# Kernel tuning notes

Hardware: AMD Instinct MI355X
Metric: run time of the kernel (lower is better)

## Reference

```python
import jax, jax.numpy as jnp
import numpy as np

L, H, NH, NKV, HD, I, MAXS = 5, 1024, 16, 8, 128, 3072, 16
EPS = 1e-6
THETA = 1000000.0
N_REP = NH // NKV


def rms(x, w, eps=EPS):
    # RMSNorm over last dim (fp32 math as in the torch module)
    return w * (x * jax.lax.rsqrt(jnp.mean(x * x, axis=-1, keepdims=True) + eps))


def rotate_half(v):
    d = v.shape[-1] // 2
    return jnp.concatenate([-v[..., d:], v[..., :d]], axis=-1)


def setup_inputs() -> dict:
    key = jax.random.key(0)
    ks = jax.random.split(key, 20)
    s = 0.02
    inp = {
        'hidden_states': jax.random.normal(ks[0], (1, 1, H), jnp.float32),
        'position_id': jax.random.randint(ks[1], (1,), 0, MAXS, jnp.int64) if jax.config.jax_enable_x64 else jax.random.randint(ks[1], (1,), 0, MAXS).astype(jnp.int32),
        'past_keys': jax.random.normal(ks[2], (L, 1, NKV, MAXS, HD), jnp.float32),
        'past_values': jax.random.normal(ks[3], (L, 1, NKV, MAXS, HD), jnp.float32),
        'w_iln': jnp.ones((L, H), jnp.float32),
        'w_paln': jnp.ones((L, H), jnp.float32),
        'wq': jax.random.normal(ks[4], (L, NH * HD, H), jnp.float32) * s,
        'wk': jax.random.normal(ks[5], (L, NKV * HD, H), jnp.float32) * s,
        'wv': jax.random.normal(ks[6], (L, NKV * HD, H), jnp.float32) * s,
        'wo': jax.random.normal(ks[7], (L, H, NH * HD), jnp.float32) * s,
        'w_qn': jnp.ones((L, HD), jnp.float32),
        'w_kn': jnp.ones((L, HD), jnp.float32),
        'w_gate': jax.random.normal(ks[8], (L, I, H), jnp.float32) * s,
        'w_up': jax.random.normal(ks[9], (L, I, H), jnp.float32) * s,
        'w_down': jax.random.normal(ks[10], (L, H, I), jnp.float32) * s,
        'w_onorm': jnp.ones((H,), jnp.float32),
    }
    return inp


def reference(hidden_states, position_id, past_keys, past_values,
              w_iln, w_paln, wq, wk, wv, wo, w_qn, w_kn,
              w_gate, w_up, w_down, w_onorm):
    pos = position_id[0]
    # RoPE tables at the single decode position
    inv_freq = 1.0 / (THETA ** (jnp.arange(0, HD, 2, dtype=jnp.float32) / HD))  # [HD/2]
    freqs = pos.astype(jnp.float32) * inv_freq
    cos = jnp.concatenate([jnp.cos(freqs)] * 2)  # [HD]
    sin = jnp.concatenate([jnp.sin(freqs)] * 2)
    mask = jnp.arange(MAXS) > pos  # [MAXS] future positions masked
    scale = 1.0 / jnp.sqrt(jnp.float32(HD))

    x = hidden_states[0, 0]  # [H]

    def layer(x, xs):
        pk, pv, wi, wp, q_, k_, v_, o_, qn, kn, g_, u_, d_ = xs
        h = rms(x, wi)
        q = (q_ @ h).reshape(NH, HD)
        k_new = rms((k_ @ h).reshape(NKV, HD), kn)
        v_new = (v_ @ h).reshape(NKV, HD)
        q = rms(q, qn)
        q = q * cos + rotate_half(q) * sin
        k_new = k_new * cos + rotate_half(k_new) * sin
        # write new K/V at pos into the fixed-size cache
        kc = pk[0].at[:, pos, :].set(k_new)  # [NKV, MAXS, HD]
        vc = pv[0].at[:, pos, :].set(v_new)
        # GQA: repeat each kv head N_REP times (contiguous, matching torch expand)
        ke = jnp.repeat(kc, N_REP, axis=0)  # [NH, MAXS, HD]
        ve = jnp.repeat(vc, N_REP, axis=0)
        scores = jnp.einsum('hd,hkd->hk', q, ke) * scale
        scores = jnp.where(mask[None, :], -jnp.inf, scores)
        p = jax.nn.softmax(scores, axis=-1)
        attn = jnp.einsum('hk,hkd->hd', p, ve).reshape(NH * HD)
        x = x + o_ @ attn
        h = rms(x, wp)
        x = x + d_ @ (jax.nn.silu(g_ @ h) * (u_ @ h))
        return x, (kc[None], vc[None])

    xs = (past_keys, past_values, w_iln, w_paln, wq, wk, wv, wo,
          w_qn, w_kn, w_gate, w_up, w_down)
    x, (pks, pvs) = jax.lax.scan(layer, x, xs)
    out = rms(x, w_onorm)[None, None, :]  # [1,1,H]
    return out, pks, pvs


if __name__ == '__main__':
    o = reference(**setup_inputs())
    print(o[0].shape, o[1].shape, o[2].shape)
```

## Files before the change

kernel.cpp:

```cpp
#include <hip/hip_runtime.h>
#include <hip/hip_bf16.h>
#include <math.h>

typedef __hip_bfloat16 bf16;

#define L_    5
#define H_    1024
#define NH_   16
#define NKV_  8
#define HD_   128
#define I_    3072
#define MAXS_ 16
#define EPS_  1e-6f
#define KVE_  (L_ * NKV_ * MAXS_ * HD_)

static __device__ __forceinline__ float bl(unsigned u){ return __uint_as_float(u << 16); }
static __device__ __forceinline__ float bh(unsigned u){ return __uint_as_float(u & 0xffff0000u); }
static __device__ __forceinline__ float b2f(bf16 v){ return __bfloat162float(v); }

static __device__ __forceinline__ float wred(float v){
#pragma unroll
    for (int o = 32; o; o >>= 1) v += __shfl_xor(v, o, 64);
    return v;
}

static __device__ __forceinline__ float dot8(uint4 u, float4 a, float4 b){
    return bl(u.x)*a.x + bh(u.x)*a.y + bl(u.y)*a.z + bh(u.y)*a.w
         + bl(u.z)*b.x + bh(u.z)*b.y + bl(u.w)*b.z + bh(u.w)*b.w;
}

static __device__ __forceinline__ float rms_inv(float sumsq, float n){
    float a = sumsq / n + EPS_;
    float y = rsqrtf(a);
    y = y * (1.5f - 0.5f * a * y * y);
    return y;
}

static __device__ __forceinline__ float ld1(const void* p, size_t i, bool b16){
    return b16 ? b2f(((const bf16*)p)[i]) : ((const float*)p)[i];
}
static __device__ __forceinline__ void st1(void* p, size_t i, float v, bool b16){
    if (b16) ((bf16*)p)[i] = __float2bfloat16(v);
    else     ((float*)p)[i] = v;
}

static __device__ __forceinline__ float rowdot(const void* w, size_t off, int n,
                                               const float* hs, bool b16, int lane){
    float acc = 0.f;
    if (b16) {
        const uint4* wp = (const uint4*)((const ushort*)w + off);
#pragma unroll 6
        for (int c = 0; c < n / 512; c++) {
            uint4 u = wp[c * 64 + lane];
            const float4* h4 = (const float4*)&hs[c * 512 + lane * 8];
            acc += dot8(u, h4[0], h4[1]);
        }
    } else {
        const float4* wp = (const float4*)((const float*)w + off);
#pragma unroll 12
        for (int c = 0; c < n / 256; c++) {
            float4 u = wp[c * 64 + lane];
            float4 h = *(const float4*)&hs[c * 256 + lane * 4];
            acc += u.x * h.x + u.y * h.y + u.z * h.z + u.w * h.w;
        }
    }
    return acc;
}

__global__ void k_probe(const void* __restrict__ w_onorm, int* __restrict__ flag){
    if (threadIdx.x == 0 && blockIdx.x == 0)
        flag[0] = (((const ushort*)w_onorm)[0] == 0x3F80) ? 1 : 0;
}

__global__ __launch_bounds__(256) void k_init(const void* __restrict__ hid,
                                              const void* __restrict__ pk,
                                              const void* __restrict__ pv,
                                              const int* __restrict__ flag,
                                              float* __restrict__ x,
                                              void* __restrict__ out){
    bool b16 = flag[0] != 0;
    int i = blockIdx.x * 256 + threadIdx.x;
    if (i < H_) x[i] = ld1(hid, i, b16);
    if (b16) {
        const int NV = KVE_ / 8;
        if (i < NV) {
            ((uint4*)((bf16*)out + H_))[i]        = ((const uint4*)pk)[i];
            ((uint4*)((bf16*)out + H_ + KVE_))[i] = ((const uint4*)pv)[i];
        }
    } else {
        const int NV = KVE_ / 4;
        if (i < NV) {
            ((uint4*)((float*)out + H_))[i]        = ((const uint4*)pk)[i];
            ((uint4*)((float*)out + H_ + KVE_))[i] = ((const uint4*)pv)[i];
        }
    }
}

__global__ __launch_bounds__(256) void k_qkv(const float* __restrict__ x,
                                             const void* __restrict__ w_iln,
                                             const void* __restrict__ wq,
                                             const void* __restrict__ wk,
                                             const void* __restrict__ wv,
                                             const int* __restrict__ flag,
                                             float* __restrict__ qraw,
                                             float* __restrict__ kraw,
                                             float* __restrict__ vraw,
                                             int layer){
    __shared__ float hs[H_];
    __shared__ float red[4];
    bool b16 = flag[0] != 0;
    int tid = threadIdx.x, lane = tid & 63, wid = tid >> 6;

    float ss = 0.f;
    for (int j = tid; j < H_; j += 256) { float xv = x[j]; ss += xv * xv; hs[j] = xv; }
    ss = wred(ss);
    if (lane == 0) red[wid] = ss;
    __syncthreads();
    float inv = rms_inv(red[0] + red[1] + red[2] + red[3], (float)H_);
    for (int j = tid; j < H_; j += 256) hs[j] = hs[j] * inv * ld1(w_iln, (size_t)layer * H_ + j, b16);
    __syncthreads();

    for (int rr = wid; rr < 8; rr += 4) {
        int r = blockIdx.x * 8 + rr;
        const void* w; size_t off; float* dst;
        if (r < NH_ * HD_) {
            w = wq; off = (size_t)layer * NH_ * HD_ * H_ + (size_t)r * H_; dst = qraw + r;
        } else if (r < NH_ * HD_ + NKV_ * HD_) {
            int rk = r - NH_ * HD_;
            w = wk; off = (size_t)layer * NKV_ * HD_ * H_ + (size_t)rk * H_; dst = kraw + rk;
        } else {
            int rv = r - NH_ * HD_ - NKV_ * HD_;
            w = wv; off = (size_t)layer * NKV_ * HD_ * H_ + (size_t)rv * H_; dst = vraw + rv;
        }
        float acc = wred(rowdot(w, off, H_, hs, b16, lane));
        if (lane == 0) *dst = acc;
    }
}

__global__ __launch_bounds__(64) void k_rope(const float* __restrict__ qraw,
                                             const float* __restrict__ kraw,
                                             const float* __restrict__ vraw,
                                             const void* __restrict__ w_qn,
                                             const void* __restrict__ w_kn,
                                             const int* __restrict__ pos_p,
                                             const int* __restrict__ flag,
                                             float* __restrict__ qrot,
                                             void* __restrict__ out,
                                             int layer){
    bool b16 = flag[0] != 0;
    int b = blockIdx.x, lane = threadIdx.x;
    int pos = pos_p[0];
    pos = pos < 0 ? 0 : (pos > MAXS_ - 1 ? MAXS_ - 1 : pos);

    float fr = (float)pos * exp2f(-(float)lane * 0.31143075889569023f);
    float c = cosf(fr), s = sinf(fr);

    if (b < NH_) {
        int hh = b;
        float q0 = qraw[hh * HD_ + lane], q1 = qraw[hh * HD_ + 64 + lane];
        float inv = rms_inv(wred(q0 * q0 + q1 * q1), (float)HD_);
        q0 = q0 * inv * ld1(w_qn, (size_t)layer * HD_ + lane, b16);
        q1 = q1 * inv * ld1(w_qn, (size_t)layer * HD_ + 64 + lane, b16);
        qrot[hh * HD_ + lane]      = q0 * c - q1 * s;
        qrot[hh * HD_ + 64 + lane] = q1 * c + q0 * s;
    } else {
        int g = b - NH_;
        float k0 = kraw[g * HD_ + lane], k1 = kraw[g * HD_ + 64 + lane];
        float inv = rms_inv(wred(k0 * k0 + k1 * k1), (float)HD_);
        k0 = k0 * inv * ld1(w_kn, (size_t)layer * HD_ + lane, b16);
        k1 = k1 * inv * ld1(w_kn, (size_t)layer * HD_ + 64 + lane, b16);
        float k0r = k0 * c - k1 * s;
        float k1r = k1 * c + k0 * s;
        size_t kco = H_ + (size_t)layer * NKV_ * MAXS_ * HD_ + (size_t)g * MAXS_ * HD_;
        size_t vco = kco + KVE_;
        st1(out, kco + pos * HD_ + lane,      k0r, b16);
        st1(out, kco + pos * HD_ + 64 + lane, k1r, b16);
        st1(out, vco + pos * HD_ + lane,      vraw[g * HD_ + lane], b16);
        st1(out, vco + pos * HD_ + 64 + lane, vraw[g * HD_ + 64 + lane], b16);
    }
}

__global__ __launch_bounds__(64) void k_attn(const float* __restrict__ qrot,
                                             const int* __restrict__ pos_p,
                                             const int* __restrict__ flag,
                                             float* __restrict__ attn,
                                             const void* __restrict__ out,
                                             int layer){
    bool b16 = flag[0] != 0;
    int hh = blockIdx.x, lane = threadIdx.x, g = hh >> 1;
    int pos = pos_p[0];
    pos = pos < 0 ? 0 : (pos > MAXS_ - 1 ? MAXS_ - 1 : pos);

    size_t kco = H_ + (size_t)layer * NKV_ * MAXS_ * HD_ + (size_t)g * MAXS_ * HD_;
    size_t vco = kco + KVE_;

    float q0 = qrot[hh * HD_ + lane], q1 = qrot[hh * HD_ + 64 + lane];
    const float scale = 0.08838834764831845f;

    float sc[MAXS_];
    float m = -3.0e38f;
#pragma unroll
    for (int t = 0; t < MAXS_; t++) {
        float d = q0 * ld1(out, kco + t * HD_ + lane, b16)
                + q1 * ld1(out, kco + t * HD_ + 64 + lane, b16);
        d = wred(d) * scale;
        sc[t] = d;
        if (t <= pos) m = fmaxf(m, d);
    }
    float se = 0.f;
    float p[MAXS_];
#pragma unroll
    for (int t = 0; t < MAXS_; t++) {
        float e = (t <= pos) ? expf(sc[t] - m) : 0.0f;
        p[t] = e;
        se += e;
    }
    float rinv = 1.0f / se;
    float a0 = 0.f, a1 = 0.f;
#pragma unroll
    for (int t = 0; t < MAXS_; t++) {
        float pt = p[t] * rinv;
        a0 += pt * ld1(out, vco + t * HD_ + lane, b16);
        a1 += pt * ld1(out, vco + t * HD_ + 64 + lane, b16);
    }
    attn[hh * HD_ + lane]      = a0;
    attn[hh * HD_ + 64 + lane] = a1;
}

__global__ __launch_bounds__(256) void k_oproj(const float* __restrict__ attn,
                                               const void* __restrict__ wo,
                                               const int* __restrict__ flag,
                                               float* __restrict__ x,
                                               int layer){
    __shared__ float as_[NH_ * HD_];
    bool b16 = flag[0] != 0;
    int tid = threadIdx.x, lane = tid & 63, wid = tid >> 6;
    for (int j = tid; j < NH_ * HD_; j += 256) as_[j] = attn[j];
    __syncthreads();
    for (int rr = wid; rr < 8; rr += 4) {
        int r = blockIdx.x * 8 + rr;
        size_t off = (size_t)layer * H_ * NH_ * HD_ + (size_t)r * NH_ * HD_;
        float acc = wred(rowdot(wo, off, NH_ * HD_, as_, b16, lane));
        if (lane == 0) x[r] += acc;
    }
}

__global__ __launch_bounds__(256) void k_gateup(const float* __restrict__ x,
                                                const void* __restrict__ w_paln,
                                                const void* __restrict__ w_gate,
                                                const void* __restrict__ w_up,
                                                const int* __restrict__ flag,
                                                float* __restrict__ act,
                                                int layer){
    __shared__ float hs[H_];
    __shared__ float red[4];
    bool b16 = flag[0] != 0;
    int tid = threadIdx.x, lane = tid & 63, wid = tid >> 6;

    float ss = 0.f;
    for (int j = tid; j < H_; j += 256) { float xv = x[j]; ss += xv * xv; hs[j] = xv; }
    ss = wred(ss);
    if (lane == 0) red[wid] = ss;
    __syncthreads();
    float inv = rms_inv(red[0] + red[1] + red[2] + red[3], (float)H_);
    for (int j = tid; j < H_; j += 256) hs[j] = hs[j] * inv * ld1(w_paln, (size_t)layer * H_ + j, b16);
    __syncthreads();

    for (int pp = wid; pp < 8; pp += 4) {
        int i = blockIdx.x * 8 + pp;
        size_t off = (size_t)layer * I_ * H_ + (size_t)i * H_;
        float ag = wred(rowdot(w_gate, off, H_, hs, b16, lane));
        float au = wred(rowdot(w_up,   off, H_, hs, b16, lane));
        if (lane == 0) {
            float sig = 1.0f / (1.0f + expf(-ag));
            act[i] = ag * sig * au;
        }
    }
}

__global__ __launch_bounds__(256) void k_down(const float* __restrict__ act,
                                              const void* __restrict__ w_down,
                                              const int* __restrict__ flag,
                                              float* __restrict__ x,
                                              int layer){
    __shared__ float as_[I_];
    bool b16 = flag[0] != 0;
    int tid = threadIdx.x, lane = tid & 63, wid = tid >> 6;
    for (int j = tid; j < I_; j += 256) as_[j] = act[j];
    __syncthreads();
    for (int rr = wid; rr < 8; rr += 4) {
        int r = blockIdx.x * 8 + rr;
        size_t off = (size_t)layer * H_ * I_ + (size_t)r * I_;
        float acc = wred(rowdot(w_down, off, I_, as_, b16, lane));
        if (lane == 0) x[r] += acc;
    }
}

__global__ __launch_bounds__(256) void k_final(const float* __restrict__ x,
                                               const void* __restrict__ w_onorm,
                                               const int* __restrict__ flag,
                                               void* __restrict__ out){
    __shared__ float red[4];
    bool b16 = flag[0] != 0;
    int tid = threadIdx.x, lane = tid & 63, wid = tid >> 6;
    float ss = 0.f;
    for (int j = tid; j < H_; j += 256) { float xv = x[j]; ss += xv * xv; }
    ss = wred(ss);
    if (lane == 0) red[wid] = ss;
    __syncthreads();
    float inv = rms_inv(red[0] + red[1] + red[2] + red[3], (float)H_);
    for (int j = tid; j < H_; j += 256)
        st1(out, j, x[j] * inv * ld1(w_onorm, j, b16), b16);
}

extern "C" void kernel_launch(void* const* d_in, const int* in_sizes, int n_in,
                              void* d_out, int out_size, void* d_ws, size_t ws_size,
                              hipStream_t stream) {
    const void* hid     = d_in[0];
    const int*  pos     = (const int*)d_in[1];
    const void* pk      = d_in[2];
    const void* pv      = d_in[3];
    const void* w_iln   = d_in[4];
    const void* w_paln  = d_in[5];
    const void* wq      = d_in[6];
    const void* wk      = d_in[7];
    const void* wv      = d_in[8];
    const void* wo      = d_in[9];
    const void* w_qn    = d_in[10];
    const void* w_kn    = d_in[11];
    const void* w_gate  = d_in[12];
    const void* w_up    = d_in[13];
    const void* w_down  = d_in[14];
    const void* w_onorm = d_in[15];

    float* ws   = (float*)d_ws;
    int*   flag = (int*)ws;
    float* x    = ws + 16;
    float* qraw = x + 1024;
    float* kraw = qraw + 2048;
    float* vraw = kraw + 1024;
    float* qrot = vraw + 1024;
    float* attn = qrot + 2048;
    float* act  = attn + 2048;

    k_probe<<<1, 64, 0, stream>>>(w_onorm, flag);
    k_init<<<80, 256, 0, stream>>>(hid, pk, pv, flag, x, d_out);
    for (int l = 0; l < L_; l++) {
        k_qkv<<<512, 256, 0, stream>>>(x, w_iln, wq, wk, wv, flag, qraw, kraw, vraw, l);
        k_rope<<<24, 64, 0, stream>>>(qraw, kraw, vraw, w_qn, w_kn, pos, flag, qrot, d_out, l);
        k_attn<<<16, 64, 0, stream>>>(qrot, pos, flag, attn, d_out, l);
        k_oproj<<<128, 256, 0, stream>>>(attn, wo, flag, x, l);
        k_gateup<<<384, 256, 0, stream>>>(x, w_paln, w_gate, w_up, flag, act, l);
        k_down<<<128, 256, 0, stream>>>(act, w_down, flag, x, l);
    }
    k_final<<<1, 256, 0, stream>>>(x, w_onorm, flag, d_out);
}
```

Before: 475.3 us.

## Fuse all decode layers into one cooperative persistent kernel with grid syncs

```diff
diff --git a/kernel.cpp b/kernel.cpp
--- a/kernel.cpp
+++ b/kernel.cpp
@@ -1,7 +1,9 @@
 #include <hip/hip_runtime.h>
+#include <hip/hip_cooperative_groups.h>
 #include <hip/hip_bf16.h>
 #include <math.h>
 
+namespace cg = cooperative_groups;
 typedef __hip_bfloat16 bf16;
 
 #define L_    5
@@ -49,7 +51,6 @@
     float acc = 0.f;
     if (b16) {
         const uint4* wp = (const uint4*)((const ushort*)w + off);
-#pragma unroll 6
         for (int c = 0; c < n / 512; c++) {
             uint4 u = wp[c * 64 + lane];
             const float4* h4 = (const float4*)&hs[c * 512 + lane * 8];
@@ -57,7 +58,6 @@
         }
     } else {
         const float4* wp = (const float4*)((const float*)w + off);
-#pragma unroll 12
         for (int c = 0; c < n / 256; c++) {
             float4 u = wp[c * 64 + lane];
             float4 h = *(const float4*)&hs[c * 256 + lane * 4];
@@ -65,6 +65,193 @@
         }
     }
     return acc;
+}
+
+struct MArgs {
+    const void *hid, *pk, *pv, *w_iln, *w_paln, *wq, *wk, *wv, *wo;
+    const void *w_qn, *w_kn, *w_gate, *w_up, *w_down, *w_onorm;
+    const int* pos;
+    float *x, *qraw, *kraw, *vraw, *attn, *act;
+    void* out;
+};
+
+__global__ __launch_bounds__(256, 2) void k_mega(MArgs a){
+    cg::grid_group grid = cg::this_grid();
+    __shared__ float smem[I_];
+    __shared__ float red4[4];
+    __shared__ float pA[16], pB[16];
+    const bool b16 = (((const ushort*)a.w_onorm)[0] == 0x3F80);
+    const int tid = threadIdx.x, lane = tid & 63, wid = tid >> 6;
+    const int b = blockIdx.x;
+    const int gsz = gridDim.x * 256, gtid = b * 256 + tid;
+    int pos = a.pos[0]; pos = pos < 0 ? 0 : (pos > MAXS_ - 1 ? MAXS_ - 1 : pos);
+
+    for (int i = gtid; i < H_; i += gsz) a.x[i] = ld1(a.hid, i, b16);
+    if (b16) {
+        uint4* ko = (uint4*)((bf16*)a.out + H_);
+        uint4* vo = (uint4*)((bf16*)a.out + H_ + KVE_);
+        for (int i = gtid; i < KVE_ / 8; i += gsz) { ko[i] = ((const uint4*)a.pk)[i]; vo[i] = ((const uint4*)a.pv)[i]; }
+    } else {
+        uint4* ko = (uint4*)((float*)a.out + H_);
+        uint4* vo = (uint4*)((float*)a.out + H_ + KVE_);
+        for (int i = gtid; i < KVE_ / 4; i += gsz) { ko[i] = ((const uint4*)a.pk)[i]; vo[i] = ((const uint4*)a.pv)[i]; }
+    }
+    grid.sync();
+
+    for (int l = 0; l < L_; l++) {
+        {
+            float ss = 0.f;
+            for (int j = tid; j < H_; j += 256) { float xv = a.x[j]; ss += xv * xv; smem[j] = xv; }
+            ss = wred(ss);
+            if (lane == 0) red4[wid] = ss;
+            __syncthreads();
+            float inv = rms_inv(red4[0] + red4[1] + red4[2] + red4[3], (float)H_);
+            for (int j = tid; j < H_; j += 256) smem[j] = smem[j] * inv * ld1(a.w_iln, (size_t)l * H_ + j, b16);
+            __syncthreads();
+            for (int rr = wid; rr < 8; rr += 4) {
+                int r = b * 8 + rr;
+                const void* w; size_t off; float* dst;
+                if (r < NH_ * HD_) {
+                    w = a.wq; off = (size_t)l * NH_ * HD_ * H_ + (size_t)r * H_; dst = a.qraw + r;
+                } else if (r < NH_ * HD_ + NKV_ * HD_) {
+                    int rk = r - NH_ * HD_;
+                    w = a.wk; off = (size_t)l * NKV_ * HD_ * H_ + (size_t)rk * H_; dst = a.kraw + rk;
+                } else {
+                    int rv = r - NH_ * HD_ - NKV_ * HD_;
+                    w = a.wv; off = (size_t)l * NKV_ * HD_ * H_ + (size_t)rv * H_; dst = a.vraw + rv;
+                }
+                float acc = wred(rowdot(w, off, H_, smem, b16, lane));
+                if (lane == 0) *dst = acc;
+            }
+        }
+        grid.sync();
+
+        {
+            int gw = b * 4 + wid;
+            if (gw < NH_ + NKV_) {
+                float fr = (float)pos * exp2f(-(float)lane * 0.31143075889569023f);
+                float c = cosf(fr), s = sinf(fr);
+                if (gw < NH_) {
+                    int hh = gw, g = hh >> 1;
+                    float q0 = a.qraw[hh * HD_ + lane], q1 = a.qraw[hh * HD_ + 64 + lane];
+                    float inv = rms_inv(wred(q0 * q0 + q1 * q1), (float)HD_);
+                    q0 = q0 * inv * ld1(a.w_qn, (size_t)l * HD_ + lane, b16);
+                    q1 = q1 * inv * ld1(a.w_qn, (size_t)l * HD_ + 64 + lane, b16);
+                    float q0r = q0 * c - q1 * s, q1r = q1 * c + q0 * s;
+                    float k0 = a.kraw[g * HD_ + lane], k1 = a.kraw[g * HD_ + 64 + lane];
+                    inv = rms_inv(wred(k0 * k0 + k1 * k1), (float)HD_);
+                    k0 = k0 * inv * ld1(a.w_kn, (size_t)l * HD_ + lane, b16);
+                    k1 = k1 * inv * ld1(a.w_kn, (size_t)l * HD_ + 64 + lane, b16);
+                    float k0r = k0 * c - k1 * s, k1r = k1 * c + k0 * s;
+                    float v0 = a.vraw[g * HD_ + lane], v1 = a.vraw[g * HD_ + 64 + lane];
+
+                    size_t kco = H_ + (size_t)l * NKV_ * MAXS_ * HD_ + (size_t)g * MAXS_ * HD_;
+                    size_t vco = kco + KVE_;
+                    const float scale = 0.08838834764831845f;
+                    float sc[MAXS_]; float m = -3.0e38f;
+#pragma unroll
+                    for (int t = 0; t < MAXS_; t++) {
+                        float d = (t == pos) ? (q0r * k0r + q1r * k1r)
+                                             : (q0r * ld1(a.out, kco + t * HD_ + lane, b16)
+                                              + q1r * ld1(a.out, kco + t * HD_ + 64 + lane, b16));
+                        d = wred(d) * scale;
+                        sc[t] = d;
+                        if (t <= pos) m = fmaxf(m, d);
+                    }
+                    float se = 0.f; float p[MAXS_];
+#pragma unroll
+                    for (int t = 0; t < MAXS_; t++) { float e = (t <= pos) ? expf(sc[t] - m) : 0.0f; p[t] = e; se += e; }
+                    float rinv = 1.0f / se;
+                    float a0 = 0.f, a1 = 0.f;
+#pragma unroll
+                    for (int t = 0; t < MAXS_; t++) {
+                        float pt = p[t] * rinv;
+                        float w0 = (t == pos) ? v0 : ld1(a.out, vco + t * HD_ + lane, b16);
+                        float w1 = (t == pos) ? v1 : ld1(a.out, vco + t * HD_ + 64 + lane, b16);
+                        a0 += pt * w0; a1 += pt * w1;
+                    }
+                    a.attn[hh * HD_ + lane] = a0;
+                    a.attn[hh * HD_ + 64 + lane] = a1;
+                } else {
+                    int g = gw - NH_;
+                    float k0 = a.kraw[g * HD_ + lane], k1 = a.kraw[g * HD_ + 64 + lane];
+                    float inv = rms_inv(wred(k0 * k0 + k1 * k1), (float)HD_);
+                    k0 = k0 * inv * ld1(a.w_kn, (size_t)l * HD_ + lane, b16);
+                    k1 = k1 * inv * ld1(a.w_kn, (size_t)l * HD_ + 64 + lane, b16);
+                    float k0r = k0 * c - k1 * s, k1r = k1 * c + k0 * s;
+                    size_t kco = H_ + (size_t)l * NKV_ * MAXS_ * HD_ + (size_t)g * MAXS_ * HD_;
+                    size_t vco = kco + KVE_;
+                    st1(a.out, kco + pos * HD_ + lane,      k0r, b16);
+                    st1(a.out, kco + pos * HD_ + 64 + lane, k1r, b16);
+                    st1(a.out, vco + pos * HD_ + lane,      a.vraw[g * HD_ + lane], b16);
+                    st1(a.out, vco + pos * HD_ + 64 + lane, a.vraw[g * HD_ + 64 + lane], b16);
+                }
+            }
+        }
+        grid.sync();
+
+        {
+            for (int j = tid; j < NH_ * HD_; j += 256) smem[j] = a.attn[j];
+            __syncthreads();
+            int r = b * 2 + (wid >> 1), h = wid & 1;
+            size_t off = (size_t)l * H_ * NH_ * HD_ + (size_t)r * NH_ * HD_ + (size_t)h * 1024;
+            float acc = wred(rowdot(a.wo, off, 1024, smem + h * 1024, b16, lane));
+            if (lane == 0) pA[wid] = acc;
+            __syncthreads();
+            if (tid < 2) a.x[b * 2 + tid] += pA[2 * tid] + pA[2 * tid + 1];
+        }
+        grid.sync();
+
+        {
+            float ss = 0.f;
+            for (int j = tid; j < H_; j += 256) { float xv = a.x[j]; ss += xv * xv; smem[j] = xv; }
+            ss = wred(ss);
+            if (lane == 0) red4[wid] = ss;
+            __syncthreads();
+            float inv = rms_inv(red4[0] + red4[1] + red4[2] + red4[3], (float)H_);
+            for (int j = tid; j < H_; j += 256) smem[j] = smem[j] * inv * ld1(a.w_paln, (size_t)l * H_ + j, b16);
+            __syncthreads();
+            for (int k = wid * 3; k < wid * 3 + 3; k++) {
+                int j = k >> 1, h = k & 1;
+                int i = b * 6 + j;
+                size_t off = (size_t)l * I_ * H_ + (size_t)i * H_ + (size_t)h * 512;
+                float ag = wred(rowdot(a.w_gate, off, 512, smem + h * 512, b16, lane));
+                float au = wred(rowdot(a.w_up,   off, 512, smem + h * 512, b16, lane));
+                if (lane == 0) { pA[k] = ag; pB[k] = au; }
+            }
+            __syncthreads();
+            if (tid < 6) {
+                float ag = pA[2 * tid] + pA[2 * tid + 1];
+                float au = pB[2 * tid] + pB[2 * tid + 1];
+                float sig = 1.0f / (1.0f + expf(-ag));
+                a.act[b * 6 + tid] = ag * sig * au;
+            }
+        }
+        grid.sync();
+
+        {
+            for (int j = tid; j < I_; j += 256) smem[j] = a.act[j];
+            __syncthreads();
+            int r = b * 2 + (wid >> 1), h = wid & 1;
+            size_t off = (size_t)l * H_ * I_ + (size_t)r * I_ + (size_t)h * 1536;
+            float acc = wred(rowdot(a.w_down, off, 1536, smem + h * 1536, b16, lane));
+            if (lane == 0) pA[wid] = acc;
+            __syncthreads();
+            if (tid < 2) a.x[b * 2 + tid] += pA[2 * tid] + pA[2 * tid + 1];
+        }
+        grid.sync();
+    }
+
+    if (b == 0) {
+        float ss = 0.f;
+        for (int j = tid; j < H_; j += 256) { float xv = a.x[j]; ss += xv * xv; }
+        ss = wred(ss);
+        if (lane == 0) red4[wid] = ss;
+        __syncthreads();
+        float inv = rms_inv(red4[0] + red4[1] + red4[2] + red4[3], (float)H_);
+        for (int j = tid; j < H_; j += 256)
+            st1(a.out, j, a.x[j] * inv * ld1(a.w_onorm, j, b16), b16);
+    }
 }
 
 __global__ void k_probe(const void* __restrict__ w_onorm, int* __restrict__ flag){
@@ -110,7 +297,6 @@
     __shared__ float red[4];
     bool b16 = flag[0] != 0;
     int tid = threadIdx.x, lane = tid & 63, wid = tid >> 6;
-
     float ss = 0.f;
     for (int j = tid; j < H_; j += 256) { float xv = x[j]; ss += xv * xv; hs[j] = xv; }
     ss = wred(ss);
@@ -119,7 +305,6 @@
     float inv = rms_inv(red[0] + red[1] + red[2] + red[3], (float)H_);
     for (int j = tid; j < H_; j += 256) hs[j] = hs[j] * inv * ld1(w_iln, (size_t)layer * H_ + j, b16);
     __syncthreads();
-
     for (int rr = wid; rr < 8; rr += 4) {
         int r = blockIdx.x * 8 + rr;
         const void* w; size_t off; float* dst;
@@ -151,10 +336,8 @@
     int b = blockIdx.x, lane = threadIdx.x;
     int pos = pos_p[0];
     pos = pos < 0 ? 0 : (pos > MAXS_ - 1 ? MAXS_ - 1 : pos);
-
     float fr = (float)pos * exp2f(-(float)lane * 0.31143075889569023f);
     float c = cosf(fr), s = sinf(fr);
-
     if (b < NH_) {
         int hh = b;
         float q0 = qraw[hh * HD_ + lane], q1 = qraw[hh * HD_ + 64 + lane];
@@ -190,13 +373,10 @@
     int hh = blockIdx.x, lane = threadIdx.x, g = hh >> 1;
     int pos = pos_p[0];
     pos = pos < 0 ? 0 : (pos > MAXS_ - 1 ? MAXS_ - 1 : pos);
-
     size_t kco = H_ + (size_t)layer * NKV_ * MAXS_ * HD_ + (size_t)g * MAXS_ * HD_;
     size_t vco = kco + KVE_;
-
     float q0 = qrot[hh * HD_ + lane], q1 = qrot[hh * HD_ + 64 + lane];
     const float scale = 0.08838834764831845f;
-
     float sc[MAXS_];
     float m = -3.0e38f;
 #pragma unroll
@@ -256,7 +436,6 @@
     __shared__ float red[4];
     bool b16 = flag[0] != 0;
     int tid = threadIdx.x, lane = tid & 63, wid = tid >> 6;
-
     float ss = 0.f;
     for (int j = tid; j < H_; j += 256) { float xv = x[j]; ss += xv * xv; hs[j] = xv; }
     ss = wred(ss);
@@ -265,7 +444,6 @@
     float inv = rms_inv(red[0] + red[1] + red[2] + red[3], (float)H_);
     for (int j = tid; j < H_; j += 256) hs[j] = hs[j] * inv * ld1(w_paln, (size_t)layer * H_ + j, b16);
     __syncthreads();
-
     for (int pp = wid; pp < 8; pp += 4) {
         int i = blockIdx.x * 8 + pp;
         size_t off = (size_t)layer * I_ * H_ + (size_t)i * H_;
@@ -343,15 +521,26 @@
     float* attn = qrot + 2048;
     float* act  = attn + 2048;
 
-    k_probe<<<1, 64, 0, stream>>>(w_onorm, flag);
-    k_init<<<80, 256, 0, stream>>>(hid, pk, pv, flag, x, d_out);
-    for (int l = 0; l < L_; l++) {
-        k_qkv<<<512, 256, 0, stream>>>(x, w_iln, wq, wk, wv, flag, qraw, kraw, vraw, l);
-        k_rope<<<24, 64, 0, stream>>>(qraw, kraw, vraw, w_qn, w_kn, pos, flag, qrot, d_out, l);
-        k_attn<<<16, 64, 0, stream>>>(qrot, pos, flag, attn, d_out, l);
-        k_oproj<<<128, 256, 0, stream>>>(attn, wo, flag, x, l);
-        k_gateup<<<384, 256, 0, stream>>>(x, w_paln, w_gate, w_up, flag, act, l);
-        k_down<<<128, 256, 0, stream>>>(act, w_down, flag, x, l);
-    }
-    k_final<<<1, 256, 0, stream>>>(x, w_onorm, flag, d_out);
-}
+    MArgs ma;
+    ma.hid = hid; ma.pk = pk; ma.pv = pv; ma.w_iln = w_iln; ma.w_paln = w_paln;
+    ma.wq = wq; ma.wk = wk; ma.wv = wv; ma.wo = wo; ma.w_qn = w_qn; ma.w_kn = w_kn;
+    ma.w_gate = w_gate; ma.w_up = w_up; ma.w_down = w_down; ma.w_onorm = w_onorm;
+    ma.pos = pos; ma.x = x; ma.qraw = qraw; ma.kraw = kraw; ma.vraw = vraw;
+    ma.attn = attn; ma.act = act; ma.out = d_out;
+    void* kp[] = { &ma };
+    hipError_t err = hipLaunchCooperativeKernel((const void*)k_mega, dim3(512), dim3(256),
+                                                kp, 0, stream);
+    if (err != hipSuccess) {
+        k_probe<<<1, 64, 0, stream>>>(w_onorm, flag);
+        k_init<<<80, 256, 0, stream>>>(hid, pk, pv, flag, x, d_out);
+        for (int l = 0; l < L_; l++) {
+            k_qkv<<<512, 256, 0, stream>>>(x, w_iln, wq, wk, wv, flag, qraw, kraw, vraw, l);
+            k_rope<<<24, 64, 0, stream>>>(qraw, kraw, vraw, w_qn, w_kn, pos, flag, qrot, d_out, l);
+            k_attn<<<16, 64, 0, stream>>>(qrot, pos, flag, attn, d_out, l);
+            k_oproj<<<128, 256, 0, stream>>>(attn, wo, flag, x, l);
+            k_gateup<<<384, 256, 0, stream>>>(x, w_paln, w_gate, w_up, flag, act, l);
+            k_down<<<128, 256, 0, stream>>>(act, w_down, flag, x, l);
+        }
+        k_final<<<1, 256, 0, stream>>>(x, w_onorm, flag, d_out);
+    }
+}
```

New measurement: 1.790 ms. 277% more time.
